# Performance work log

Measured on AMD Instinct MI355X. Metric: run time of the kernel, lower is better.

The kernel has to match this reference:

```python
import jax, jax.numpy as jnp
import numpy as np

EPS = 1e-8  # torch.nn.CosineSimilarity default eps


def setup_inputs() -> dict:
    key = jax.random.key(0)
    k1, k2 = jax.random.split(key)
    N, C, K = 131072, 128, 512
    embeddings = jax.random.normal(k1, (N, C), dtype=jnp.float32)
    prototypes = jax.random.normal(k2, (K, C), dtype=jnp.float32)
    return {"embeddings": embeddings, "prototypes": prototypes}


def reference(embeddings, prototypes):
    # Cosine similarity between each embedding and each prototype, expressed as
    # a normalized GEMM instead of the O(N*K*C) broadcast the torch code builds.
    e = embeddings / jnp.maximum(
        jnp.linalg.norm(embeddings, axis=-1, keepdims=True), EPS)
    p = prototypes / jnp.maximum(
        jnp.linalg.norm(prototypes, axis=-1, keepdims=True), EPS)
    cos = jnp.einsum('nc,kc->nk', e, p)  # (N, K)
    dists = 1.0 - cos
    scores = -(dists * dists)
    return scores
```

## Files before the change

### kernel.cpp

```cpp
#include <hip/hip_runtime.h>

#define EPS_F 1e-8f

typedef float  f32x4  __attribute__((ext_vector_type(4)));
typedef __bf16 bf16x8 __attribute__((ext_vector_type(8)));
typedef unsigned short u16x4 __attribute__((ext_vector_type(4)));

__device__ inline unsigned short f2bf(float x) {
  unsigned int u = __float_as_uint(x);
  u += 0x7fffu + ((u >> 16) & 1u);
  return (unsigned short)(u >> 16);
}

__global__ __launch_bounds__(256) void proto_norm_kernel(
    const float* __restrict__ proto, unsigned short* __restrict__ Bn)
{
  const int tid = threadIdx.x;
  const int g   = tid & 31;
  const int row = blockIdx.x * 8 + (tid >> 5);
  const float4 v = *(const float4*)&proto[row * 128 + g * 4];
  float ss = v.x*v.x + v.y*v.y + v.z*v.z + v.w*v.w;
  #pragma unroll
  for (int m = 16; m >= 1; m >>= 1) ss += __shfl_xor(ss, m);
  const float rn = 1.0f / fmaxf(sqrtf(ss), EPS_F);
  u16x4 b;
  b[0] = f2bf(v.x * rn); b[1] = f2bf(v.y * rn);
  b[2] = f2bf(v.z * rn); b[3] = f2bf(v.w * rn);
  *(u16x4*)&Bn[row * 128 + g * 4] = b;
}

__global__ __launch_bounds__(256) void hproto_kernel(
    const float* __restrict__ emb, const unsigned short* __restrict__ Bn,
    float* __restrict__ out)
{
  constexpr int CD = 128;
  constexpr int KP = 512;
  constexpr int BM = 128;

  __shared__ unsigned short sA[BM * CD];
  __shared__ float rne[BM];

  const int tid  = threadIdx.x;
  const int lane = tid & 63;
  const int wave = tid >> 6;
  const long brow = (long)blockIdx.x * BM;

  {
    const float4* s4 = (const float4*)(emb + brow * CD);
    #pragma unroll
    for (int s = 0; s < 16; ++s) {
      int f  = s * 256 + tid;
      int r  = f >> 5;
      int c4 = f & 31;
      float4 v = s4[f];
      float ss = v.x*v.x + v.y*v.y + v.z*v.z + v.w*v.w;
      #pragma unroll
      for (int m = 16; m >= 1; m >>= 1) ss += __shfl_xor(ss, m);
      if ((tid & 31) == 0) rne[r] = 1.0f / fmaxf(sqrtf(ss), EPS_F);
      u16x4 b;
      b[0] = f2bf(v.x); b[1] = f2bf(v.y); b[2] = f2bf(v.z); b[3] = f2bf(v.w);
      int idx = (r * CD + c4 * 4) ^ ((r & 7) << 3);
      *(u16x4*)&sA[idx] = b;
    }
  }
  __syncthreads();

  const int wr = (wave >> 1) * 64;
  const int wc = (wave & 1) * 64;
  const int hi = lane >> 4;
  const int lo = lane & 15;

  f32x4 re[4];
  #pragma unroll
  for (int m = 0; m < 4; ++m)
    re[m] = *(const f32x4*)&rne[wr + m * 16 + hi * 4];

  float* const obase = out + (brow + wr + hi * 4) * KP + wc + lo;

  #pragma unroll 1
  for (int c = 0; c < 4; ++c) {
    bf16x8 bfr[4][4];
    #pragma unroll
    for (int n = 0; n < 4; ++n) {
      const unsigned short* bp = Bn + (c * 128 + wc + n * 16 + lo) * CD + hi * 8;
      #pragma unroll
      for (int kk = 0; kk < 4; ++kk)
        bfr[kk][n] = *(const bf16x8*)(bp + kk * 32);
    }

    f32x4 acc[4][4];
    #pragma unroll
    for (int m = 0; m < 4; ++m)
      #pragma unroll
      for (int n = 0; n < 4; ++n) acc[m][n] = f32x4{0.f, 0.f, 0.f, 0.f};

    #pragma unroll
    for (int kk = 0; kk < 4; ++kk) {
      const int k0 = kk * 32 + hi * 8;
      bf16x8 af[4];
      #pragma unroll
      for (int m = 0; m < 4; ++m) {
        int row = wr + m * 16 + lo;
        int idx = (row * CD + k0) ^ ((row & 7) << 3);
        af[m] = *(const bf16x8*)&sA[idx];
      }
      #pragma unroll
      for (int m = 0; m < 4; ++m)
        #pragma unroll
        for (int n = 0; n < 4; ++n)
          acc[m][n] = __builtin_amdgcn_mfma_f32_16x16x32_bf16(af[m], bfr[kk][n], acc[m][n], 0, 0, 0);
    }

    float* const oc = obase + c * 128;
    #pragma unroll
    for (int m = 0; m < 4; ++m) {
      #pragma unroll
      for (int j = 0; j < 4; ++j) {
        float* orow = oc + (long)(m * 16 + j) * KP;
        #pragma unroll
        for (int n = 0; n < 4; ++n) {
          float cs = acc[m][n][j] * re[m][j];
          float d  = 1.0f - cs;
          __builtin_nontemporal_store(-(d * d), orow + n * 16);
        }
      }
    }
  }
}

extern "C" void kernel_launch(void* const* d_in, const int* in_sizes, int n_in,
                              void* d_out, int out_size, void* d_ws, size_t ws_size,
                              hipStream_t stream) {
  const float* emb   = (const float*)d_in[0];
  const float* proto = (const float*)d_in[1];
  float* out = (float*)d_out;
  unsigned short* Bn = (unsigned short*)d_ws;
  const int C = 128;
  const int N = in_sizes[0] / C;
  const int K = in_sizes[1] / C;
  proto_norm_kernel<<<K / 8, 256, 0, stream>>>(proto, Bn);
  hproto_kernel<<<N / 128, 256, 0, stream>>>(emb, Bn, out);
}
```

Before: 342.8 us.

## Keep A fragments in registers, drop LDS staging, double-buffer B loads

Each wave now loads its own 32 embedding rows straight from global memory into MFMA A-fragments, computing row norms with two shuffles, which removes the shared-memory tile and the block barrier. The prototype matrix is streamed in 32-column slices with register double-buffering so the next slice's global loads overlap the current MFMAs. Operands are swapped so each lane writes contiguous float4 outputs instead of scalar stores, and launch bounds request three blocks per CU. The per-wave tile shrinks from 64x64 to 32x32, so B is re-read from cache more often and there is less MFMA work to hide load latency.

```diff
diff --git a/kernel.cpp b/kernel.cpp
--- a/kernel.cpp
+++ b/kernel.cpp
@@ -5,6 +5,7 @@
 typedef float  f32x4  __attribute__((ext_vector_type(4)));
 typedef __bf16 bf16x8 __attribute__((ext_vector_type(8)));
 typedef unsigned short u16x4 __attribute__((ext_vector_type(4)));
+typedef unsigned short u16x8 __attribute__((ext_vector_type(8)));
 
 __device__ inline unsigned short f2bf(float x) {
   unsigned int u = __float_as_uint(x);
@@ -29,102 +30,97 @@
   *(u16x4*)&Bn[row * 128 + g * 4] = b;
 }
 
-__global__ __launch_bounds__(256) void hproto_kernel(
+__global__ __launch_bounds__(256, 3) void hproto_kernel(
     const float* __restrict__ emb, const unsigned short* __restrict__ Bn,
     float* __restrict__ out)
 {
   constexpr int CD = 128;
   constexpr int KP = 512;
-  constexpr int BM = 128;
-
-  __shared__ unsigned short sA[BM * CD];
-  __shared__ float rne[BM];
 
   const int tid  = threadIdx.x;
   const int lane = tid & 63;
   const int wave = tid >> 6;
-  const long brow = (long)blockIdx.x * BM;
+  const int lo   = lane & 15;
+  const int hi   = lane >> 4;
+  const long rbase = (long)blockIdx.x * 128 + wave * 32;
 
-  {
-    const float4* s4 = (const float4*)(emb + brow * CD);
+  bf16x8 bufA[2][4], bufB[2][4];
+  auto loadB = [&](bf16x8 (&dst)[2][4], int s) {
+    const unsigned short* bp = Bn + (s * 32 + lo) * CD + hi * 8;
     #pragma unroll
-    for (int s = 0; s < 16; ++s) {
-      int f  = s * 256 + tid;
-      int r  = f >> 5;
-      int c4 = f & 31;
-      float4 v = s4[f];
-      float ss = v.x*v.x + v.y*v.y + v.z*v.z + v.w*v.w;
+    for (int n = 0; n < 2; ++n)
       #pragma unroll
-      for (int m = 16; m >= 1; m >>= 1) ss += __shfl_xor(ss, m);
-      if ((tid & 31) == 0) rne[r] = 1.0f / fmaxf(sqrtf(ss), EPS_F);
-      u16x4 b;
-      b[0] = f2bf(v.x); b[1] = f2bf(v.y); b[2] = f2bf(v.z); b[3] = f2bf(v.w);
-      int idx = (r * CD + c4 * 4) ^ ((r & 7) << 3);
-      *(u16x4*)&sA[idx] = b;
+      for (int kk = 0; kk < 4; ++kk)
+        dst[n][kk] = *(const bf16x8*)(bp + n * 16 * CD + kk * 32);
+  };
+
+  loadB(bufA, 0);
+
+  bf16x8 af[2][4];
+  float  re[2];
+  #pragma unroll
+  for (int m = 0; m < 2; ++m) {
+    const float* rp = emb + (rbase + m * 16 + lo) * CD + hi * 8;
+    f32x4 a[4][2];
+    #pragma unroll
+    for (int kk = 0; kk < 4; ++kk) {
+      a[kk][0] = *(const f32x4*)(rp + kk * 32);
+      a[kk][1] = *(const f32x4*)(rp + kk * 32 + 4);
     }
+    float ss = 0.f;
+    #pragma unroll
+    for (int kk = 0; kk < 4; ++kk) {
+      u16x8 b;
+      #pragma unroll
+      for (int j = 0; j < 4; ++j) {
+        ss += a[kk][0][j] * a[kk][0][j] + a[kk][1][j] * a[kk][1][j];
+        b[j]     = f2bf(a[kk][0][j]);
+        b[4 + j] = f2bf(a[kk][1][j]);
+      }
+      af[m][kk] = __builtin_bit_cast(bf16x8, b);
+    }
+    ss += __shfl_xor(ss, 16);
+    ss += __shfl_xor(ss, 32);
+    re[m] = 1.0f / fmaxf(sqrtf(ss), EPS_F);
   }
-  __syncthreads();
 
-  const int wr = (wave >> 1) * 64;
-  const int wc = (wave & 1) * 64;
-  const int hi = lane >> 4;
-  const int lo = lane & 15;
+  float* const ob = out + (rbase + lo) * KP + hi * 4;
 
-  f32x4 re[4];
-  #pragma unroll
-  for (int m = 0; m < 4; ++m)
-    re[m] = *(const f32x4*)&rne[wr + m * 16 + hi * 4];
-
-  float* const obase = out + (brow + wr + hi * 4) * KP + wc + lo;
+  auto compute = [&](bf16x8 (&buf)[2][4], int s) {
+    f32x4 acc[2][2];
+    #pragma unroll
+    for (int m = 0; m < 2; ++m)
+      #pragma unroll
+      for (int n = 0; n < 2; ++n) acc[m][n] = f32x4{0.f, 0.f, 0.f, 0.f};
+    #pragma unroll
+    for (int kk = 0; kk < 4; ++kk)
+      #pragma unroll
+      for (int m = 0; m < 2; ++m)
+        #pragma unroll
+        for (int n = 0; n < 2; ++n)
+          acc[m][n] = __builtin_amdgcn_mfma_f32_16x16x32_bf16(
+              buf[n][kk], af[m][kk], acc[m][n], 0, 0, 0);
+    #pragma unroll
+    for (int m = 0; m < 2; ++m)
+      #pragma unroll
+      for (int n = 0; n < 2; ++n) {
+        f32x4 v;
+        #pragma unroll
+        for (int j = 0; j < 4; ++j) {
+          float d = 1.0f - acc[m][n][j] * re[m];
+          v[j] = -(d * d);
+        }
+        __builtin_nontemporal_store(v, (f32x4*)(ob + m * 16 * KP + s * 32 + n * 16));
+      }
+  };
 
   #pragma unroll 1
-  for (int c = 0; c < 4; ++c) {
-    bf16x8 bfr[4][4];
-    #pragma unroll
-    for (int n = 0; n < 4; ++n) {
-      const unsigned short* bp = Bn + (c * 128 + wc + n * 16 + lo) * CD + hi * 8;
-      #pragma unroll
-      for (int kk = 0; kk < 4; ++kk)
-        bfr[kk][n] = *(const bf16x8*)(bp + kk * 32);
-    }
-
-    f32x4 acc[4][4];
-    #pragma unroll
-    for (int m = 0; m < 4; ++m)
-      #pragma unroll
-      for (int n = 0; n < 4; ++n) acc[m][n] = f32x4{0.f, 0.f, 0.f, 0.f};
-
-    #pragma unroll
-    for (int kk = 0; kk < 4; ++kk) {
-      const int k0 = kk * 32 + hi * 8;
-      bf16x8 af[4];
-      #pragma unroll
-      for (int m = 0; m < 4; ++m) {
-        int row = wr + m * 16 + lo;
-        int idx = (row * CD + k0) ^ ((row & 7) << 3);
-        af[m] = *(const bf16x8*)&sA[idx];
-      }
-      #pragma unroll
-      for (int m = 0; m < 4; ++m)
-        #pragma unroll
-        for (int n = 0; n < 4; ++n)
-          acc[m][n] = __builtin_amdgcn_mfma_f32_16x16x32_bf16(af[m], bfr[kk][n], acc[m][n], 0, 0, 0);
-    }
-
-    float* const oc = obase + c * 128;
-    #pragma unroll
-    for (int m = 0; m < 4; ++m) {
-      #pragma unroll
-      for (int j = 0; j < 4; ++j) {
-        float* orow = oc + (long)(m * 16 + j) * KP;
-        #pragma unroll
-        for (int n = 0; n < 4; ++n) {
-          float cs = acc[m][n][j] * re[m][j];
-          float d  = 1.0f - cs;
-          __builtin_nontemporal_store(-(d * d), orow + n * 16);
-        }
-      }
-    }
+  for (int t = 0; t < 8; ++t) {
+    const int s0 = t * 2;
+    loadB(bufB, s0 + 1);
+    compute(bufA, s0);
+    if (t < 7) loadB(bufA, s0 + 2);
+    compute(bufB, s0 + 1);
   }
 }
 
```

New measurement: 353.5 us. +3.1%, slower.
